# Kernel tuning notes

Hardware: AMD Instinct MI355X
Metric: run time of the kernel (lower is better)

## Reference

```python
import jax, jax.numpy as jnp
import jax.scipy.fft as jsp_fft
import numpy as np

B, NX, NY, DV = 4, 512, 512, 32
KX, KY = 64, 64


def setup_inputs() -> dict:
    key = jax.random.key(0)
    k1, k2, k3 = jax.random.split(key, 3)
    x = jax.random.normal(k1, (B, NX, NY, DV), dtype=jnp.float32)
    R_real = jax.random.uniform(k2, (DV, DV, KX, KY), dtype=jnp.float32)
    R_imag = jax.random.uniform(k3, (DV, DV, KX, KY), dtype=jnp.float32)
    return {"x": x, "R_real": R_real, "R_imag": R_imag}


def reference(x, R_real, R_imag):
    # x: [B, nX, nY, dv]
    R = R_real + 1j * R_imag  # [dv_out, dv_in, kX, kY]
    kX, kY = R.shape[-2:]
    nX = x.shape[1]

    xt = jnp.moveaxis(x, -1, -3)                      # [B, dv, nX, nY]
    xd = jsp_fft.dct(xt, type=2, axis=-1, norm='ortho')   # DCT-II along Y
    xf = jnp.fft.rfft(xd, axis=-2, norm='ortho')      # [B, dv, nX//2+1, nY] complex
    nXf, nY = xf.shape[-2:]

    # Truncation einsum with identity-padded T matrices == slicing
    xtr = xf[..., :kX, :kY]                           # [B, dv, kX, kY]
    # Per-mode complex channel mixing
    y = jnp.einsum('ijab,ejab->eiab', R, xtr)         # [B, dv, kX, kY]
    # Inverse truncation == zero-padding back to full spectrum
    yp = jnp.pad(y, ((0, 0), (0, 0), (0, nXf - kX), (0, nY - kY)))

    yr = jnp.fft.irfft(yp, n=nX, axis=-2, norm='ortho')
    yd = jsp_fft.idct(yr, type=2, axis=-1, norm='ortho')
    return jnp.moveaxis(yd, -3, -1)                   # [B, nX, nY, dv]
```

## Files before the change

kernel.cpp:

```cpp
#include <hip/hip_runtime.h>
#include <math.h>

#define BB 4
#define NXD 512
#define NYD 512
#define DVD 32
#define KXD 64
#define KYD 64

#define OFF_DN  0
#define OFF_DT  32768
#define OFF_FCN 65536
#define OFF_FSN 98304
#define OFF_FCT 131072
#define OFF_FST 163840
#define OFF_C   196608
#define OFF_FR  4390912
#define OFF_FI  4915200
#define OFF_YR  5439488
#define OFF_YI  5963776
#define OFF_G   6488064

__device__ __forceinline__ void gload_lds16(const float* g, float* l) {
    __builtin_amdgcn_global_load_lds(
        (const __attribute__((address_space(1))) void*)g,
        (__attribute__((address_space(3))) void*)l, 16, 0, 0);
}

__global__ __launch_bounds__(256) void k_tables(float* __restrict__ ws) {
    int idx = blockIdx.x * 256 + threadIdx.x;
    int k = idx >> 9;
    int n = idx & 511;
    const float inv_sq512 = 0.04419417382415922f;
    float ak = (k == 0) ? inv_sq512 : 0.0625f;
    int m = (k * (2 * n + 1)) & 2047;
    float d = ak * cospif((float)m * (1.0f / 1024.0f));
    ws[OFF_DN + k * 512 + n] = d;
    ws[OFF_DT + n * 64 + k] = d;
    int mf = (k * n) & 511;
    float c = cospif((float)mf * (1.0f / 256.0f)) * inv_sq512;
    float s = sinpif((float)mf * (1.0f / 256.0f)) * inv_sq512;
    ws[OFF_FCN + k * 512 + n] = c;
    ws[OFF_FSN + k * 512 + n] = s;
    ws[OFF_FCT + n * 64 + k] = c;
    ws[OFF_FST + n * 64 + k] = s;
}

__global__ __launch_bounds__(256) void k_dct(const float* __restrict__ x,
                                             const float* __restrict__ ws,
                                             float* __restrict__ C) {
    __shared__ __align__(16) float xs[2][2 * 2048];
    int b = blockIdx.x >> 8;
    int nx = (blockIdx.x & 255) * 2;
    int t = threadIdx.x;
    int wv = t >> 6;
    int dv0 = (t & 15) * 2;
    int ky0 = (t >> 4) * 4;
    const float* Dt = ws + OFF_DT;
    const float* xb = x + (size_t)(b * NXD + nx) * NYD * DVD;

    auto stage = [&](int buf, int ch) {
#pragma unroll
        for (int n = 0; n < 2; ++n) {
            const float* src = xb + ((size_t)n * NYD + ch * 64) * DVD;
#pragma unroll
            for (int p = 0; p < 2; ++p) {
                int f = p * 256 + t;
                gload_lds16(src + f * 4, xs[buf] + n * 2048 + (p * 256 + wv * 64) * 4);
            }
        }
    };

    float a[2][4][2] = {};
    stage(0, 0);
    __syncthreads();
    for (int ch = 0; ch < 8; ++ch) {
        int buf = ch & 1;
        if (ch < 7) stage(buf ^ 1, ch + 1);
        const float* dtc = Dt + ch * 4096 + ky0;
        const float* xsb = xs[buf];
#pragma unroll 4
        for (int nyc = 0; nyc < 64; ++nyc) {
            float4 d4 = *(const float4*)(dtc + nyc * 64);
            float2 x0 = *(const float2*)(xsb + nyc * 32 + dv0);
            float2 x1 = *(const float2*)(xsb + 2048 + nyc * 32 + dv0);
            float da[4] = {d4.x, d4.y, d4.z, d4.w};
#pragma unroll
            for (int q = 0; q < 4; ++q) {
                a[0][q][0] += da[q] * x0.x; a[0][q][1] += da[q] * x0.y;
                a[1][q][0] += da[q] * x1.x; a[1][q][1] += da[q] * x1.y;
            }
        }
        __syncthreads();
    }
#pragma unroll
    for (int n = 0; n < 2; ++n)
#pragma unroll
        for (int q = 0; q < 4; ++q) {
            float2 v; v.x = a[n][q][0]; v.y = a[n][q][1];
            *(float2*)(C + ((size_t)((b * KYD + ky0 + q) * NXD + nx + n)) * DVD + dv0) = v;
        }
}

__global__ __launch_bounds__(256) void k_rfft(const float* __restrict__ Cbuf,
                                              const float* __restrict__ ws,
                                              float* __restrict__ Fr,
                                              float* __restrict__ Fi) {
    __shared__ __align__(16) float cs[2][4096];
    int b = blockIdx.x >> 7;
    int r = blockIdx.x & 127;
    int ky = r >> 1;
    int dvbase = (r & 1) * 16;
    int t = threadIdx.x;
    int wv = t >> 6;
    int dv0 = (t & 7) * 2;
    int kx0 = (t >> 3) * 2;
    const float* Tc = ws + OFF_FCT;
    const float* Ts = ws + OFF_FST;
    const float* Cb = Cbuf + (size_t)(b * KYD + ky) * NXD * DVD + dvbase;

    auto stage = [&](int buf, int ch) {
#pragma unroll
        for (int p = 0; p < 4; ++p) {
            int fi4 = p * 256 + t;
            int row = fi4 >> 2, c4 = fi4 & 3;
            gload_lds16(Cb + (size_t)(ch * 256 + row) * DVD + c4 * 4,
                        cs[buf] + (p * 256 + wv * 64) * 4);
        }
    };

    float ar[2][2] = {}, ai[2][2] = {};
    stage(0, 0);
    __syncthreads();
    for (int ch = 0; ch < 2; ++ch) {
        if (ch == 0) stage(1, 1);
        const float* csb = cs[ch];
        int nx0 = ch * 256;
#pragma unroll 8
        for (int nxc = 0; nxc < 256; ++nxc) {
            float2 cv = *(const float2*)(csb + nxc * 16 + dv0);
            float2 c2 = *(const float2*)(Tc + (nx0 + nxc) * 64 + kx0);
            float2 s2 = *(const float2*)(Ts + (nx0 + nxc) * 64 + kx0);
            ar[0][0] += c2.x * cv.x; ar[0][1] += c2.x * cv.y;
            ar[1][0] += c2.y * cv.x; ar[1][1] += c2.y * cv.y;
            ai[0][0] -= s2.x * cv.x; ai[0][1] -= s2.x * cv.y;
            ai[1][0] -= s2.y * cv.x; ai[1][1] -= s2.y * cv.y;
        }
        __syncthreads();
    }
#pragma unroll
    for (int q = 0; q < 2; ++q) {
        size_t o = ((size_t)((b * KYD + ky) * KXD + kx0 + q)) * DVD + dvbase + dv0;
        float2 vr; vr.x = ar[q][0]; vr.y = ar[q][1];
        float2 vi; vi.x = ai[q][0]; vi.y = ai[q][1];
        *(float2*)(Fr + o) = vr;
        *(float2*)(Fi + o) = vi;
    }
}

__global__ __launch_bounds__(256) void k_mix(const float* __restrict__ Rr,
                                             const float* __restrict__ Ri,
                                             const float* __restrict__ Fr,
                                             const float* __restrict__ Fi,
                                             float* __restrict__ Yr,
                                             float* __restrict__ Yi) {
    __shared__ float fl[2 * 32 * 64 * 2];
    int kx = blockIdx.x & 63;
    int ig = (blockIdx.x >> 6) & 7;
    int eh = blockIdx.x >> 9;
    int t = threadIdx.x;
    int j = t & 31, kyb = t >> 5;
#pragma unroll
    for (int e2 = 0; e2 < 2; ++e2) {
        int e = eh * 2 + e2;
#pragma unroll
        for (int p = 0; p < 8; ++p) {
            int ky = p * 8 + kyb;
            size_t go = ((size_t)((e * KYD + ky) * KXD + kx)) * DVD + j;
            int lo = ((e2 * 32 + j) * 64 + ((ky + j) & 63)) * 2;
            fl[lo] = Fr[go];
            fl[lo + 1] = Fi[go];
        }
    }
    __syncthreads();
    int lane = t & 63, w = t >> 6;
    int i = ig * 4 + w;
    size_t rb = (size_t)(i * 32) * 4096 + kx * 64 + lane;
    float yr[2] = {}, yi[2] = {};
#pragma unroll 8
    for (int jj = 0; jj < 32; ++jj) {
        float rr = Rr[rb + (size_t)jj * 4096];
        float ri = Ri[rb + (size_t)jj * 4096];
#pragma unroll
        for (int e2 = 0; e2 < 2; ++e2) {
            float2 f = *(const float2*)(fl + ((e2 * 32 + jj) * 64 + ((lane + jj) & 63)) * 2);
            yr[e2] += rr * f.x - ri * f.y;
            yi[e2] += rr * f.y + ri * f.x;
        }
    }
#pragma unroll
    for (int e2 = 0; e2 < 2; ++e2) {
        int e = eh * 2 + e2;
        size_t o = ((size_t)((e * DVD + i) * KXD + kx)) * KYD + lane;
        Yr[o] = yr[e2];
        Yi[o] = yi[e2];
    }
}

__global__ __launch_bounds__(256) void k_irfft(const float* __restrict__ Yr,
                                               const float* __restrict__ Yi,
                                               const float* __restrict__ ws,
                                               float* __restrict__ G) {
    __shared__ __align__(16) float ylr[64 * 64];
    __shared__ __align__(16) float yli[64 * 64];
    int blk = blockIdx.x;
    int oct = blk & 7;
    int i = (blk >> 3) & 31;
    int b = blk >> 8;
    int t = threadIdx.x;
    size_t ybase = ((size_t)(b * DVD + i)) * KXD * KYD;
#pragma unroll
    for (int p = 0; p < 4; ++p) {
        int f = p * 256 + t;
        float wk = (f < 16) ? 1.0f : 2.0f;
        float4 vr = *(const float4*)(Yr + ybase + (size_t)f * 4);
        float4 vi = *(const float4*)(Yi + ybase + (size_t)f * 4);
        vr.x *= wk; vr.y *= wk; vr.z *= wk; vr.w *= wk;
        vi.x *= wk; vi.y *= wk; vi.z *= wk; vi.w *= wk;
        *(float4*)(ylr + f * 4) = vr;
        *(float4*)(yli + f * 4) = vi;
    }
    __syncthreads();
    int kyg = t & 15, nxg = t >> 4;
    int ky0 = kyg * 4;
    int gnx0 = oct * 64 + nxg * 4;
    const float* Tc = ws + OFF_FCN;
    const float* Ts = ws + OFF_FSN;
    float acc[4][4] = {};
    for (int kx = 0; kx < 64; ++kx) {
        float4 cv = *(const float4*)(Tc + kx * 512 + gnx0);
        float4 sv = *(const float4*)(Ts + kx * 512 + gnx0);
        float4 vr = *(const float4*)(ylr + kx * 64 + ky0);
        float4 vi = *(const float4*)(yli + kx * 64 + ky0);
        float ca[4] = {cv.x, cv.y, cv.z, cv.w};
        float sa[4] = {sv.x, sv.y, sv.z, sv.w};
        float ra[4] = {vr.x, vr.y, vr.z, vr.w};
        float ia[4] = {vi.x, vi.y, vi.z, vi.w};
#pragma unroll
        for (int q = 0; q < 4; ++q)
#pragma unroll
            for (int kk = 0; kk < 4; ++kk)
                acc[q][kk] += ca[q] * ra[kk] - sa[q] * ia[kk];
    }
#pragma unroll
    for (int q = 0; q < 4; ++q) {
        float4 v; v.x = acc[q][0]; v.y = acc[q][1]; v.z = acc[q][2]; v.w = acc[q][3];
        *(float4*)(G + (((size_t)(b * NXD + gnx0 + q)) * DVD + i) * KYD + ky0) = v;
    }
}

#define GST 68
__global__ __launch_bounds__(256) void k_idct(const float* __restrict__ G,
                                              const float* __restrict__ ws,
                                              float* __restrict__ out) {
    __shared__ __align__(16) float gs[2][32 * GST];
    int b = blockIdx.x >> 8;
    int nx = (blockIdx.x & 255) * 2;
    int t = threadIdx.x;
    int ig = t & 15, nyg = t >> 4;
    int i0 = ig * 2;
    const float* Dn = ws + OFF_DN;
#pragma unroll
    for (int n = 0; n < 2; ++n) {
        const float4* src = (const float4*)(G + (size_t)(b * NXD + nx + n) * DVD * KYD);
#pragma unroll
        for (int p = 0; p < 2; ++p) {
            int f = p * 256 + t;
            int i = f >> 4, ky4 = (f & 15) * 4;
            *(float4*)(gs[n] + i * GST + ky4) = src[f];
        }
    }
    __syncthreads();
    float* outb = out + ((size_t)(b * NXD + nx)) * NYD * DVD;
    for (int c = 0; c < 8; ++c) {
        const float* dnc = Dn + c * 64 + nyg * 4;
        float acc[2][4][2] = {};
#pragma unroll 2
        for (int kyc = 0; kyc < 16; ++kyc) {
            int ky0 = kyc * 4;
            float4 g00 = *(const float4*)(gs[0] + i0 * GST + ky0);
            float4 g01 = *(const float4*)(gs[0] + (i0 + 1) * GST + ky0);
            float4 g10 = *(const float4*)(gs[1] + i0 * GST + ky0);
            float4 g11 = *(const float4*)(gs[1] + (i0 + 1) * GST + ky0);
            float g0a[2][4] = {{g00.x, g00.y, g00.z, g00.w}, {g10.x, g10.y, g10.z, g10.w}};
            float g1a[2][4] = {{g01.x, g01.y, g01.z, g01.w}, {g11.x, g11.y, g11.z, g11.w}};
#pragma unroll
            for (int kk = 0; kk < 4; ++kk) {
                float4 dv = *(const float4*)(dnc + (ky0 + kk) * 512);
                float da[4] = {dv.x, dv.y, dv.z, dv.w};
#pragma unroll
                for (int q = 0; q < 4; ++q) {
                    acc[0][q][0] += da[q] * g0a[0][kk];
                    acc[0][q][1] += da[q] * g1a[0][kk];
                    acc[1][q][0] += da[q] * g0a[1][kk];
                    acc[1][q][1] += da[q] * g1a[1][kk];
                }
            }
        }
        int ny0 = c * 64 + nyg * 4;
#pragma unroll
        for (int n = 0; n < 2; ++n)
#pragma unroll
            for (int q = 0; q < 4; ++q) {
                float2 v; v.x = acc[n][q][0]; v.y = acc[n][q][1];
                *(float2*)(outb + ((size_t)n * NYD + ny0 + q) * DVD + i0) = v;
            }
    }
}

extern "C" void kernel_launch(void* const* d_in, const int* in_sizes, int n_in,
                              void* d_out, int out_size, void* d_ws, size_t ws_size,
                              hipStream_t stream) {
    const float* x  = (const float*)d_in[0];
    const float* Rr = (const float*)d_in[1];
    const float* Ri = (const float*)d_in[2];
    float* out = (float*)d_out;
    float* ws  = (float*)d_ws;
    float* C   = ws + OFF_C;
    float* Fr  = ws + OFF_FR;
    float* Fi  = ws + OFF_FI;
    float* Yr  = ws + OFF_YR;
    float* Yi  = ws + OFF_YI;
    float* G   = ws + OFF_G;

    k_tables<<<128, 256, 0, stream>>>(ws);
    k_dct<<<BB * (NXD / 2), 256, 0, stream>>>(x, ws, C);
    k_rfft<<<BB * KYD * 2, 256, 0, stream>>>(C, ws, Fr, Fi);
    k_mix<<<KXD * 8 * 2, 256, 0, stream>>>(Rr, Ri, Fr, Fi, Yr, Yi);
    k_irfft<<<BB * DVD * 8, 256, 0, stream>>>(Yr, Yi, ws, G);
    k_idct<<<BB * NXD / 2, 256, 0, stream>>>(G, ws, out);
}
```

Measured before the change: 469.3 us.

## Stage DCT basis tables in LDS and interleave rFFT twiddles

```diff
diff --git a/kernel.cpp b/kernel.cpp
--- a/kernel.cpp
+++ b/kernel.cpp
@@ -12,8 +12,7 @@
 #define OFF_DT  32768
 #define OFF_FCN 65536
 #define OFF_FSN 98304
-#define OFF_FCT 131072
-#define OFF_FST 163840
+#define OFF_FI2 131072
 #define OFF_C   196608
 #define OFF_FR  4390912
 #define OFF_FI  4915200
@@ -42,14 +41,15 @@
     float s = sinpif((float)mf * (1.0f / 256.0f)) * inv_sq512;
     ws[OFF_FCN + k * 512 + n] = c;
     ws[OFF_FSN + k * 512 + n] = s;
-    ws[OFF_FCT + n * 64 + k] = c;
-    ws[OFF_FST + n * 64 + k] = s;
+    ws[OFF_FI2 + (n * 64 + k) * 2 + 0] = c;
+    ws[OFF_FI2 + (n * 64 + k) * 2 + 1] = s;
 }
 
 __global__ __launch_bounds__(256) void k_dct(const float* __restrict__ x,
                                              const float* __restrict__ ws,
                                              float* __restrict__ C) {
-    __shared__ __align__(16) float xs[2][2 * 2048];
+    __shared__ __align__(16) float xs[2][2][1024];
+    __shared__ __align__(16) float dt[2][2048];
     int b = blockIdx.x >> 8;
     int nx = (blockIdx.x & 255) * 2;
     int t = threadIdx.x;
@@ -61,29 +61,29 @@
 
     auto stage = [&](int buf, int ch) {
 #pragma unroll
-        for (int n = 0; n < 2; ++n) {
-            const float* src = xb + ((size_t)n * NYD + ch * 64) * DVD;
-#pragma unroll
-            for (int p = 0; p < 2; ++p) {
-                int f = p * 256 + t;
-                gload_lds16(src + f * 4, xs[buf] + n * 2048 + (p * 256 + wv * 64) * 4);
-            }
-        }
+        for (int n = 0; n < 2; ++n)
+            gload_lds16(xb + (size_t)(n * 512 + ch * 32) * 32 + t * 4,
+                        &xs[buf][n][wv * 256]);
+#pragma unroll
+        for (int p = 0; p < 2; ++p)
+            gload_lds16(Dt + ch * 2048 + (p * 256 + t) * 4,
+                        &dt[buf][(p * 256 + wv * 64) * 4]);
     };
 
     float a[2][4][2] = {};
     stage(0, 0);
     __syncthreads();
-    for (int ch = 0; ch < 8; ++ch) {
+    for (int ch = 0; ch < 16; ++ch) {
         int buf = ch & 1;
-        if (ch < 7) stage(buf ^ 1, ch + 1);
-        const float* dtc = Dt + ch * 4096 + ky0;
-        const float* xsb = xs[buf];
+        if (ch < 15) stage(buf ^ 1, ch + 1);
+        const float* dtc = &dt[buf][ky0];
+        const float* x0p = &xs[buf][0][dv0];
+        const float* x1p = &xs[buf][1][dv0];
 #pragma unroll 4
-        for (int nyc = 0; nyc < 64; ++nyc) {
+        for (int nyc = 0; nyc < 32; ++nyc) {
             float4 d4 = *(const float4*)(dtc + nyc * 64);
-            float2 x0 = *(const float2*)(xsb + nyc * 32 + dv0);
-            float2 x1 = *(const float2*)(xsb + 2048 + nyc * 32 + dv0);
+            float2 x0 = *(const float2*)(x0p + nyc * 32);
+            float2 x1 = *(const float2*)(x1p + nyc * 32);
             float da[4] = {d4.x, d4.y, d4.z, d4.w};
 #pragma unroll
             for (int q = 0; q < 4; ++q) {
@@ -106,47 +106,36 @@
                                               const float* __restrict__ ws,
                                               float* __restrict__ Fr,
                                               float* __restrict__ Fi) {
-    __shared__ __align__(16) float cs[2][4096];
+    __shared__ __align__(16) float cs[256 * 16];
     int b = blockIdx.x >> 7;
     int r = blockIdx.x & 127;
     int ky = r >> 1;
     int dvbase = (r & 1) * 16;
     int t = threadIdx.x;
-    int wv = t >> 6;
     int dv0 = (t & 7) * 2;
     int kx0 = (t >> 3) * 2;
-    const float* Tc = ws + OFF_FCT;
-    const float* Ts = ws + OFF_FST;
-    const float* Cb = Cbuf + (size_t)(b * KYD + ky) * NXD * DVD + dvbase;
-
-    auto stage = [&](int buf, int ch) {
+    const float* T2 = ws + OFF_FI2;
+    float ar[2][2] = {}, ai[2][2] = {};
+    for (int ch = 0; ch < 2; ++ch) {
+        int nx0 = ch * 256;
+        __syncthreads();
 #pragma unroll
         for (int p = 0; p < 4; ++p) {
             int fi4 = p * 256 + t;
             int row = fi4 >> 2, c4 = fi4 & 3;
-            gload_lds16(Cb + (size_t)(ch * 256 + row) * DVD + c4 * 4,
-                        cs[buf] + (p * 256 + wv * 64) * 4);
-        }
-    };
-
-    float ar[2][2] = {}, ai[2][2] = {};
-    stage(0, 0);
-    __syncthreads();
-    for (int ch = 0; ch < 2; ++ch) {
-        if (ch == 0) stage(1, 1);
-        const float* csb = cs[ch];
-        int nx0 = ch * 256;
+            *(float4*)(cs + row * 16 + c4 * 4) =
+                *(const float4*)(Cbuf + ((size_t)(b * KYD + ky) * NXD + nx0 + row) * DVD + dvbase + c4 * 4);
+        }
+        __syncthreads();
 #pragma unroll 8
         for (int nxc = 0; nxc < 256; ++nxc) {
-            float2 cv = *(const float2*)(csb + nxc * 16 + dv0);
-            float2 c2 = *(const float2*)(Tc + (nx0 + nxc) * 64 + kx0);
-            float2 s2 = *(const float2*)(Ts + (nx0 + nxc) * 64 + kx0);
-            ar[0][0] += c2.x * cv.x; ar[0][1] += c2.x * cv.y;
-            ar[1][0] += c2.y * cv.x; ar[1][1] += c2.y * cv.y;
-            ai[0][0] -= s2.x * cv.x; ai[0][1] -= s2.x * cv.y;
-            ai[1][0] -= s2.y * cv.x; ai[1][1] -= s2.y * cv.y;
-        }
-        __syncthreads();
+            float2 cv = *(const float2*)(cs + nxc * 16 + dv0);
+            float4 q = *(const float4*)(T2 + ((nx0 + nxc) * 64 + kx0) * 2);
+            ar[0][0] += q.x * cv.x; ar[0][1] += q.x * cv.y;
+            ai[0][0] -= q.y * cv.x; ai[0][1] -= q.y * cv.y;
+            ar[1][0] += q.z * cv.x; ar[1][1] += q.z * cv.y;
+            ai[1][0] -= q.w * cv.x; ai[1][1] -= q.w * cv.y;
+        }
     }
 #pragma unroll
     for (int q = 0; q < 2; ++q) {
@@ -264,12 +253,25 @@
                                               const float* __restrict__ ws,
                                               float* __restrict__ out) {
     __shared__ __align__(16) float gs[2][32 * GST];
+    __shared__ __align__(16) float dn[2][4096];
     int b = blockIdx.x >> 8;
     int nx = (blockIdx.x & 255) * 2;
     int t = threadIdx.x;
+    int wv = t >> 6;
     int ig = t & 15, nyg = t >> 4;
     int i0 = ig * 2;
     const float* Dn = ws + OFF_DN;
+
+    auto stage_dn = [&](int buf, int ch) {
+#pragma unroll
+        for (int p = 0; p < 4; ++p) {
+            int f = p * 256 + t;
+            int ky = f >> 4, ny4 = (f & 15) * 4;
+            gload_lds16(Dn + ky * 512 + ch * 64 + ny4,
+                        &dn[buf][(p * 256 + wv * 64) * 4]);
+        }
+    };
+
 #pragma unroll
     for (int n = 0; n < 2; ++n) {
         const float4* src = (const float4*)(G + (size_t)(b * NXD + nx + n) * DVD * KYD);
@@ -280,10 +282,12 @@
             *(float4*)(gs[n] + i * GST + ky4) = src[f];
         }
     }
+    stage_dn(0, 0);
     __syncthreads();
     float* outb = out + ((size_t)(b * NXD + nx)) * NYD * DVD;
     for (int c = 0; c < 8; ++c) {
-        const float* dnc = Dn + c * 64 + nyg * 4;
+        int buf = c & 1;
+        if (c < 7) stage_dn(buf ^ 1, c + 1);
         float acc[2][4][2] = {};
 #pragma unroll 2
         for (int kyc = 0; kyc < 16; ++kyc) {
@@ -296,7 +300,7 @@
             float g1a[2][4] = {{g01.x, g01.y, g01.z, g01.w}, {g11.x, g11.y, g11.z, g11.w}};
 #pragma unroll
             for (int kk = 0; kk < 4; ++kk) {
-                float4 dv = *(const float4*)(dnc + (ky0 + kk) * 512);
+                float4 dv = *(const float4*)(&dn[buf][(ky0 + kk) * 64 + nyg * 4]);
                 float da[4] = {dv.x, dv.y, dv.z, dv.w};
 #pragma unroll
                 for (int q = 0; q < 4; ++q) {
@@ -315,6 +319,7 @@
                 float2 v; v.x = acc[n][q][0]; v.y = acc[n][q][1];
                 *(float2*)(outb + ((size_t)n * NYD + ny0 + q) * DVD + i0) = v;
             }
+        __syncthreads();
     }
 }
 
```

Result: faster. 405.7 us (-13.6%).
